# Kernel tuning notes

Hardware: AMD Instinct MI355X
Metric: run time of the kernel (lower is better)

The kernel has to match this reference:

```python
import jax, jax.numpy as jnp
import numpy as np

GROUPS = 8
EPS = 1e-5


def group_norm(x, gamma, beta):
    # x: [B,H,W,C]; normalize per group over (H, W, C/g)
    B, H, W, C = x.shape
    g = GROUPS
    xg = x.reshape(B, H, W, g, C // g)
    mean = jnp.mean(xg, axis=(1, 2, 4), keepdims=True)
    var = jnp.var(xg, axis=(1, 2, 4), keepdims=True)
    xg = (xg - mean) / jnp.sqrt(var + EPS)
    return gamma * xg.reshape(B, H, W, C) + beta


def setup_inputs() -> dict:
    key = jax.random.key(0)
    ks = jax.random.split(key, 6)
    B, H, W, C = 8, 64, 64, 128
    s = 1.0 / np.sqrt(C)
    return {
        "x": jax.random.normal(ks[0], (B, H, W, C), jnp.float32),
        "gamma": jnp.ones((C,), jnp.float32),
        "beta": jnp.zeros((C,), jnp.float32),
        "wq": jax.random.normal(ks[1], (C, C), jnp.float32) * s,
        "bq": jnp.zeros((C,), jnp.float32),
        "wk": jax.random.normal(ks[2], (C, C), jnp.float32) * s,
        "bk": jnp.zeros((C,), jnp.float32),
        "wv": jax.random.normal(ks[3], (C, C), jnp.float32) * s,
        "bv": jnp.zeros((C,), jnp.float32),
        "wp": jax.random.normal(ks[4], (C, C), jnp.float32) * s,
        "bp": jnp.zeros((C,), jnp.float32),
    }


def reference(x, gamma, beta, wq, bq, wk, bk, wv, bv, wp, bp):
    B, H, W, C = x.shape
    scale = jnp.asarray(C, jnp.float32) ** -0.5
    xn = group_norm(x, gamma, beta)  # note: residual uses normalized input (as in source)
    N = H * W
    xf = xn.reshape(B, N, C)
    q = xf @ wq + bq
    k = xf @ wk + bk
    v = xf @ wv + bv
    attn = jnp.einsum('bnc,bmc->bnm', q, k) * scale  # [B, N, N]
    attn = jax.nn.softmax(attn, axis=-1)
    out = jnp.einsum('bnm,bmc->bnc', attn, v)
    out = out @ wp + bp
    return (xf + out).reshape(B, H, W, C)
```

## Files before the change

kernel.cpp:

```cpp
#include <hip/hip_runtime.h>
#include <hip/hip_bf16.h>

#define B_ 8
#define N_ 4096
#define C_ 128
#define EPSV 1e-5f
#define SPLIT 2
#define KVB 64

using bf8   = __attribute__((ext_vector_type(8))) short;
using u16x8 = __attribute__((ext_vector_type(8))) ushort;
using f32x4 = __attribute__((ext_vector_type(4))) float;

__device__ __forceinline__ ushort f2b(float f) {
  __hip_bfloat16 h = __float2bfloat16(f);
  return *reinterpret_cast<ushort*>(&h);
}
__device__ __forceinline__ float b2f(ushort u) {
  union { float f; unsigned x; } t; t.x = ((unsigned)u) << 16; return t.f;
}

__device__ __forceinline__ void gll16(const void* g, void* l) {
  __builtin_amdgcn_global_load_lds((const __attribute__((address_space(1))) void*)g,
                                   (__attribute__((address_space(3))) void*)l,
                                   16, 0, 0);
}

__global__ __launch_bounds__(256) void gnw(const float* __restrict__ x,
                                           const float* __restrict__ wq,
                                           const float* __restrict__ wk,
                                           const float* __restrict__ wv,
                                           const float* __restrict__ wp,
                                           float2* __restrict__ part,
                                           ushort* __restrict__ wt) {
  if (blockIdx.y >= 64) {
    const int widx = blockIdx.y - 64;
    const float* w = (widx == 0) ? wq : (widx == 1) ? wk : (widx == 2) ? wv : wp;
    ushort* o = wt + widx * 16384;
    const int r  = blockIdx.x * 16 + (threadIdx.x >> 4);
    const int c0 = (threadIdx.x & 15) << 3;
    const float4 v0 = *reinterpret_cast<const float4*>(w + (size_t)r * C_ + c0);
    const float4 v1 = *reinterpret_cast<const float4*>(w + (size_t)r * C_ + c0 + 4);
    const float vv[8] = {v0.x, v0.y, v0.z, v0.w, v1.x, v1.y, v1.z, v1.w};
    #pragma unroll
    for (int j = 0; j < 8; ++j) {
      const int n = c0 + j;
      const int el = (r & 7) | ((((r >> 3)) ^ (n & 7)) << 3);
      o[(size_t)n * C_ + el] = f2b(vv[j]);
    }
    return;
  }
  const int bg = blockIdx.y;
  const int b = bg >> 3, g = bg & 7;
  const int chunk = blockIdx.x;
  const float* xp = x + (size_t)b * N_ * C_ + g * 16;
  float s = 0.f, s2 = 0.f;
  const int base4 = chunk * 2048;
  for (int i = threadIdx.x; i < 2048; i += 256) {
    const int idx = base4 + i;
    const int n = idx >> 2, c4 = (idx & 3) << 2;
    const float4 v = *reinterpret_cast<const float4*>(xp + (size_t)n * C_ + c4);
    s  += v.x + v.y + v.z + v.w;
    s2 += v.x*v.x + v.y*v.y + v.z*v.z + v.w*v.w;
  }
  #pragma unroll
  for (int off = 32; off; off >>= 1) { s += __shfl_down(s, off); s2 += __shfl_down(s2, off); }
  __shared__ float red[8];
  const int wid = threadIdx.x >> 6;
  if ((threadIdx.x & 63) == 0) { red[wid] = s; red[4 + wid] = s2; }
  __syncthreads();
  if (threadIdx.x == 0)
    part[bg * 8 + chunk] = make_float2(red[0]+red[1]+red[2]+red[3],
                                       red[4]+red[5]+red[6]+red[7]);
}

__device__ __forceinline__ void block_mrs(const float2* part, int b, int tid,
                                          float2* sp, float* mrs) {
  if (tid < 64) sp[tid] = part[b * 64 + tid];
  __syncthreads();
  if (tid < 8) {
    float s = 0.f, s2 = 0.f;
    #pragma unroll
    for (int c = 0; c < 8; ++c) { s += sp[tid*8+c].x; s2 += sp[tid*8+c].y; }
    const float inv = 1.f / 65536.f;
    const float m = s * inv;
    const float var = s2 * inv - m * m;
    mrs[tid*2]   = m;
    mrs[tid*2+1] = rsqrtf(var + EPSV);
  }
  __syncthreads();
}

__global__ __launch_bounds__(256) void qkv_fused(const float* __restrict__ x,
                                                 const float2* __restrict__ part,
                                                 const float* __restrict__ gamma,
                                                 const float* __restrict__ beta,
                                                 const ushort* __restrict__ wt,
                                                 const float* __restrict__ bq,
                                                 const float* __restrict__ bk,
                                                 const float* __restrict__ bv,
                                                 ushort* __restrict__ qb, ushort* __restrict__ kb,
                                                 ushort* __restrict__ vtb,
                                                 ushort* __restrict__ xnb) {
  __shared__ ushort A[64][128];
  __shared__ ushort Bt[128][128];
  __shared__ float2 sp[64];
  __shared__ float mrs[16];
  const int m0 = blockIdx.x * 64;
  const int tid = threadIdx.x;
  const int wid = tid >> 6, lane = tid & 63;
  block_mrs(part, m0 >> 12, tid, sp, mrs);
  for (int i = tid; i < 1024; i += 256) {
    const int row = i >> 4, c = (i & 15) << 3;
    const int grow = m0 + row;
    const float mm = mrs[(c >> 4) * 2], rr = mrs[(c >> 4) * 2 + 1];
    const float4 v0 = *reinterpret_cast<const float4*>(&x[(size_t)grow * C_ + c]);
    const float4 v1 = *reinterpret_cast<const float4*>(&x[(size_t)grow * C_ + c + 4]);
    const float vv[8] = {v0.x, v0.y, v0.z, v0.w, v1.x, v1.y, v1.z, v1.w};
    u16x8 u;
    #pragma unroll
    for (int j = 0; j < 8; ++j)
      u[j] = f2b((vv[j] - mm) * rr * gamma[c+j] + beta[c+j]);
    *reinterpret_cast<u16x8*>(&xnb[(size_t)grow * C_ + c]) = u;
    const int el = ((c >> 3) ^ (row & 7)) << 3;
    *reinterpret_cast<u16x8*>(&A[row][el]) = u;
  }
  const int wm = wid >> 1, wn = wid & 1;
  const int lr = lane & 15, lk = lane >> 4;
  const float qscale = 0.12751749f;

  #pragma unroll 1
  for (int j = 0; j < 3; ++j) {
    const ushort* wtj = wt + j * 16384;
    const float* bias = (j == 0) ? bq : (j == 1) ? bk : bv;
    __syncthreads();
    {
      ushort* bt0 = &Bt[0][0];
      #pragma unroll
      for (int c8 = 0; c8 < 8; ++c8) {
        const int ch = wid * 8 + c8;
        gll16(wtj + ch * 512 + lane * 8, bt0 + ch * 512);
      }
    }
    __syncthreads();
    f32x4 acc[2][4] = {};
    #pragma unroll
    for (int ks = 0; ks < 4; ++ks) {
      const int g0 = ks * 4 + lk;
      bf8 af[2], bfv[4];
      #pragma unroll
      for (int mi = 0; mi < 2; ++mi) {
        const int row = wm * 32 + mi * 16 + lr;
        af[mi] = *reinterpret_cast<const bf8*>(&A[row][(g0 ^ (row & 7)) << 3]);
      }
      #pragma unroll
      for (int ni = 0; ni < 4; ++ni) {
        const int n = wn * 64 + ni * 16 + lr;
        bfv[ni] = *reinterpret_cast<const bf8*>(&Bt[n][(g0 ^ (n & 7)) << 3]);
      }
      #pragma unroll
      for (int mi = 0; mi < 2; ++mi)
        #pragma unroll
        for (int ni = 0; ni < 4; ++ni)
          acc[mi][ni] = __builtin_amdgcn_mfma_f32_16x16x32_bf16(af[mi], bfv[ni], acc[mi][ni], 0, 0, 0);
    }
    if (j < 2) {
      ushort* out = (j == 0) ? qb : kb;
      const float sc = (j == 0) ? qscale : 1.0f;
      #pragma unroll
      for (int mi = 0; mi < 2; ++mi)
        #pragma unroll
        for (int ni = 0; ni < 4; ++ni)
          #pragma unroll
          for (int r = 0; r < 4; ++r) {
            const int row = m0 + wm * 32 + mi * 16 + lk * 4 + r;
            const int col = wn * 64 + ni * 16 + lr;
            out[(size_t)row * C_ + col] = f2b((acc[mi][ni][r] + bias[col]) * sc);
          }
    } else {
      #pragma unroll
      for (int mi = 0; mi < 2; ++mi)
        #pragma unroll
        for (int ni = 0; ni < 4; ++ni) {
          const int rowb = m0 + wm * 32 + mi * 16 + lk * 4;
          const int col  = wn * 64 + ni * 16 + lr;
          const int bb = rowb >> 12, nn = rowb & 4095;
          const int o  = nn & 63;
          const int op = (o & 0x23) | ((o & 0x0C) << 1) | ((o & 0x10) >> 2);
          const int nnp = (nn & ~63) | op;
          const float bv2 = bias[col];
          ushort4 u;
          u.x = f2b(acc[mi][ni][0] + bv2);
          u.y = f2b(acc[mi][ni][1] + bv2);
          u.z = f2b(acc[mi][ni][2] + bv2);
          u.w = f2b(acc[mi][ni][3] + bv2);
          *reinterpret_cast<ushort4*>(&vtb[((size_t)bb * C_ + col) * N_ + nnp]) = u;
        }
    }
  }
}

__global__ __launch_bounds__(256, 2) void attn_fwd(const ushort* __restrict__ q,
                                                   const ushort* __restrict__ k,
                                                   const ushort* __restrict__ vt,
                                                   ushort* __restrict__ Op,
                                                   float* __restrict__ lsum) {
  extern __shared__ ushort smem[];
  const int bid = blockIdx.x;
  const int b   = bid & 7;
  const int qi  = (bid >> 3) & 31;
  const int z   = bid >> 8;
  const int q0  = qi * 128;
  const int tid = threadIdx.x;
  const int w = tid >> 6, lane = tid & 63;
  const int lr = lane & 15, lk = lane >> 4;
  const ushort* qb = q  + (size_t)b * N_ * C_;
  const ushort* kb = k  + (size_t)b * N_ * C_;
  const ushort* vb = vt + (size_t)b * C_ * N_;

  bf8 qf[2][4];
  #pragma unroll
  for (int h = 0; h < 2; ++h) {
    const int qrow = q0 + w * 32 + h * 16 + lr;
    #pragma unroll
    for (int ks = 0; ks < 4; ++ks)
      qf[h][ks] = *reinterpret_cast<const bf8*>(&qb[(size_t)qrow * C_ + ks * 32 + lk * 8]);
  }

  bf8 onesf;
  #pragma unroll
  for (int j = 0; j < 8; ++j) onesf[j] = (short)0x3F80;

  f32x4 oacc[2][8] = {};
  f32x4 accl[2] = {};

  const int t0 = z * 32;
  const int t1 = t0 + 32;

  const ushort* kg[4];
  const ushort* vg[4];
  #pragma unroll
  for (int j = 0; j < 4; ++j) {
    const int m = w * 4 + j;
    const int krow = m * 4 + (lane >> 4);
    kg[j] = kb + (size_t)(t0 * KVB + krow) * C_ + (((lane & 15) ^ (krow & 7)) << 3);
    const int vrow = m * 8 + (lane >> 3);
    vg[j] = vb + (size_t)vrow * N_ + t0 * KVB + (((lane & 7) ^ (vrow & 7)) << 3);
  }

  auto STAGE = [&](int sel) {
    ushort* Kd = smem + sel * 8192;
    ushort* Vd = smem + 16384 + sel * 8192;
    #pragma unroll
    for (int j = 0; j < 4; ++j) {
      const int m = w * 4 + j;
      gll16(kg[j], Kd + m * 512);
      gll16(vg[j], Vd + m * 512);
    }
    #pragma unroll
    for (int j = 0; j < 4; ++j) { kg[j] += KVB * C_; vg[j] += KVB; }
  };

  STAGE(0);
  __builtin_amdgcn_s_setprio(1);
  #pragma unroll 1
  for (int kt = t0; kt < t1; ++kt) {
    const int cur = (kt - t0) & 1;
    __syncthreads();
    if (kt + 1 < t1) STAGE(cur ^ 1);

    const ushort* Kc = smem + cur * 8192;
    const ushort* Vc = smem + 16384 + cur * 8192;

    f32x4 s[2][4] = {};
    #pragma unroll
    for (int ks = 0; ks < 4; ++ks) {
      const int g0 = ks * 4 + lk;
      bf8 kf[4];
      #pragma unroll
      for (int ni = 0; ni < 4; ++ni) {
        const int n = ni * 16 + lr;
        kf[ni] = *reinterpret_cast<const bf8*>(&Kc[n * 128 + ((g0 ^ (n & 7)) << 3)]);
      }
      #pragma unroll
      for (int h = 0; h < 2; ++h)
        #pragma unroll
        for (int ni = 0; ni < 4; ++ni)
          s[h][ni] = __builtin_amdgcn_mfma_f32_16x16x32_bf16(kf[ni], qf[h][ks], s[h][ni], 0, 0, 0);
    }

    bf8 pa[2][2];
    #pragma unroll
    for (int kss = 0; kss < 2; ++kss)
      #pragma unroll
      for (int h = 0; h < 2; ++h) {
        bf8 t;
        #pragma unroll
        for (int hi = 0; hi < 2; ++hi) {
          const f32x4 sv = s[h][kss * 2 + hi];
          #pragma unroll
          for (int r = 0; r < 4; ++r)
            t[hi * 4 + r] = (short)f2b(__builtin_amdgcn_exp2f(sv[r]));
        }
        pa[kss][h] = t;
      }
    #pragma unroll
    for (int kss = 0; kss < 2; ++kss)
      #pragma unroll
      for (int h = 0; h < 2; ++h)
        accl[h] = __builtin_amdgcn_mfma_f32_16x16x32_bf16(pa[kss][h], onesf, accl[h], 0, 0, 0);

    bf8 vf[8];
    #pragma unroll
    for (int ni = 0; ni < 8; ++ni) {
      const int d = ni * 16 + lr;
      vf[ni] = *reinterpret_cast<const bf8*>(&Vc[d * 64 + ((lk ^ (d & 7)) << 3)]);
    }
    #pragma unroll
    for (int kss = 0; kss < 2; ++kss) {
      #pragma unroll
      for (int h = 0; h < 2; ++h)
        #pragma unroll
        for (int ni = 0; ni < 8; ++ni)
          oacc[h][ni] = __builtin_amdgcn_mfma_f32_16x16x32_bf16(pa[kss][h], vf[ni], oacc[h][ni], 0, 0, 0);
      if (kss == 0) {
        #pragma unroll
        for (int ni = 0; ni < 8; ++ni) {
          const int d = ni * 16 + lr;
          vf[ni] = *reinterpret_cast<const bf8*>(&Vc[d * 64 + (((4 + lk) ^ (d & 7)) << 3)]);
        }
      }
    }
  }
  __builtin_amdgcn_s_setprio(0);

  const size_t zb = (size_t)(z * B_ + b);
  if (lr == 0) {
    #pragma unroll
    for (int h = 0; h < 2; ++h)
      #pragma unroll
      for (int r = 0; r < 4; ++r)
        lsum[zb * N_ + q0 + w * 32 + h * 16 + lk * 4 + r] = accl[h][r];
  }
  ushort* ob = Op + zb * N_ * C_;
  #pragma unroll
  for (int h = 0; h < 2; ++h)
    #pragma unroll
    for (int ni = 0; ni < 8; ++ni)
      #pragma unroll
      for (int r = 0; r < 4; ++r) {
        const int row = q0 + w * 32 + h * 16 + lk * 4 + r;
        ob[(size_t)row * C_ + ni * 16 + lr] = f2b(oacc[h][ni][r]);
      }
}

__global__ __launch_bounds__(256) void proj_res(const ushort* __restrict__ Op,
                                                const float* __restrict__ lsum,
                                                const ushort* __restrict__ wtp,
                                                const float* __restrict__ bias,
                                                const ushort* __restrict__ xnb,
                                                float* __restrict__ outp) {
  __shared__ ushort A[64][128];
  __shared__ ushort Bt[128][128];
  const int m0 = blockIdx.x * 64;
  const int tid = threadIdx.x;
  const int wid = tid >> 6, lane = tid & 63;
  const size_t BN = (size_t)B_ * N_;
  {
    ushort* bt0 = &Bt[0][0];
    #pragma unroll
    for (int c8 = 0; c8 < 8; ++c8) {
      const int ch = wid * 8 + c8;
      gll16(wtp + ch * 512 + lane * 8, bt0 + ch * 512);
    }
  }
  for (int i = tid; i < 1024; i += 256) {
    const int row = i >> 4, c = (i & 15) << 3;
    const size_t grow = m0 + row;
    float l = 0.f;
    #pragma unroll
    for (int zz = 0; zz < SPLIT; ++zz) l += lsum[zz * BN + grow];
    const float inv = 1.f / l;
    float acc8[8] = {};
    #pragma unroll
    for (int zz = 0; zz < SPLIT; ++zz) {
      const u16x8 a = *reinterpret_cast<const u16x8*>(&Op[(zz * BN + grow) * C_ + c]);
      #pragma unroll
      for (int j = 0; j < 8; ++j) acc8[j] += b2f(a[j]);
    }
    u16x8 u;
    #pragma unroll
    for (int j = 0; j < 8; ++j) u[j] = f2b(acc8[j] * inv);
    const int el = ((c >> 3) ^ (row & 7)) << 3;
    *reinterpret_cast<u16x8*>(&A[row][el]) = u;
  }
  __syncthreads();
  const int wm = wid >> 1, wn = wid & 1;
  const int lr = lane & 15, lk = lane >> 4;
  f32x4 acc[2][4] = {};
  #pragma unroll
  for (int ks = 0; ks < 4; ++ks) {
    const int g0 = ks * 4 + lk;
    bf8 af[2], bfv[4];
    #pragma unroll
    for (int mi = 0; mi < 2; ++mi) {
      const int row = wm * 32 + mi * 16 + lr;
      af[mi] = *reinterpret_cast<const bf8*>(&A[row][(g0 ^ (row & 7)) << 3]);
    }
    #pragma unroll
    for (int ni = 0; ni < 4; ++ni) {
      const int n = wn * 64 + ni * 16 + lr;
      bfv[ni] = *reinterpret_cast<const bf8*>(&Bt[n][(g0 ^ (n & 7)) << 3]);
    }
    #pragma unroll
    for (int mi = 0; mi < 2; ++mi)
      #pragma unroll
      for (int ni = 0; ni < 4; ++ni)
        acc[mi][ni] = __builtin_amdgcn_mfma_f32_16x16x32_bf16(af[mi], bfv[ni], acc[mi][ni], 0, 0, 0);
  }
  #pragma unroll
  for (int mi = 0; mi < 2; ++mi)
    #pragma unroll
    for (int ni = 0; ni < 4; ++ni) {
      const int col = wn * 64 + ni * 16 + lr;
      const float bia = bias[col];
      #pragma unroll
      for (int r = 0; r < 4; ++r) {
        const int row = m0 + wm * 32 + mi * 16 + lk * 4 + r;
        const float xn = b2f(xnb[(size_t)row * C_ + col]);
        outp[(size_t)row * C_ + col] = xn + acc[mi][ni][r] + bia;
      }
    }
}

extern "C" void kernel_launch(void* const* d_in, const int* in_sizes, int n_in,
                              void* d_out, int out_size, void* d_ws, size_t ws_size,
                              hipStream_t stream) {
  const float* x     = (const float*)d_in[0];
  const float* gamma = (const float*)d_in[1];
  const float* beta  = (const float*)d_in[2];
  const float* wq    = (const float*)d_in[3];
  const float* bq    = (const float*)d_in[4];
  const float* wk    = (const float*)d_in[5];
  const float* bk    = (const float*)d_in[6];
  const float* wv    = (const float*)d_in[7];
  const float* bv    = (const float*)d_in[8];
  const float* wp    = (const float*)d_in[9];
  const float* bp    = (const float*)d_in[10];
  float* outp = (float*)d_out;

  char* ws = (char*)d_ws;
  const size_t MB8 = (size_t)B_ * N_ * C_ * 2;
  float2* part = (float2*)(ws + 512);
  ushort* qb   = (ushort*)(ws + 8192);
  ushort* kb   = (ushort*)(ws + 8192 + MB8);
  ushort* vtb  = (ushort*)(ws + 8192 + 2*MB8);
  ushort* Op   = (ushort*)(ws + 8192 + 3*MB8);
  float*  lsum = (float*)(ws + 8192 + (3 + SPLIT)*MB8);
  ushort* wt   = (ushort*)(ws + 8192 + (3 + SPLIT)*MB8 + (size_t)SPLIT*B_*N_*4);
  ushort* xnb  = (ushort*)(ws + 8192 + (3 + SPLIT)*MB8 + (size_t)SPLIT*B_*N_*4
                           + 4 * 16384 * sizeof(ushort));

  gnw<<<dim3(8, 68), 256, 0, stream>>>(x, wq, wk, wv, wp, part, wt);
  qkv_fused<<<512, 256, 0, stream>>>(x, part, gamma, beta, wt,
                                     bq, bk, bv, qb, kb, vtb, xnb);
  (void)hipFuncSetAttribute((const void*)attn_fwd,
                            hipFuncAttributeMaxDynamicSharedMemorySize, 65536);
  attn_fwd<<<dim3(32 * B_ * SPLIT), 256, 65536, stream>>>(qb, kb, vtb, Op, lsum);
  proj_res<<<512, 256, 0, stream>>>(Op, lsum, wt + 3 * 16384, bp, xnb, outp);
}
```

Measured before the change: 96.41 us.

## Shrink attention KV tile, split keys three ways, stage output via LDS

The attention kernel now uses 32-key tiles with half the LDS per stage, targets three blocks per CU, and splits the key range into three parts instead of two so more blocks are in flight. The V-transpose permutation in the QKV kernel and the LDS swizzle for V are rewritten to match the 32-wide tiles. Output tiles are written through a swizzled LDS buffer so the global stores are 16-byte and coalesced. The trade-off is more synchronisation per key, more partial results for proj_res to combine, and tighter register limits.

```diff
diff --git a/kernel.cpp b/kernel.cpp
--- a/kernel.cpp
+++ b/kernel.cpp
@@ -5,8 +5,8 @@
 #define N_ 4096
 #define C_ 128
 #define EPSV 1e-5f
-#define SPLIT 2
-#define KVB 64
+#define SPLIT 3
+#define KVB 32
 
 using bf8   = __attribute__((ext_vector_type(8))) short;
 using u16x8 = __attribute__((ext_vector_type(8))) ushort;
@@ -185,9 +185,9 @@
           const int rowb = m0 + wm * 32 + mi * 16 + lk * 4;
           const int col  = wn * 64 + ni * 16 + lr;
           const int bb = rowb >> 12, nn = rowb & 4095;
-          const int o  = nn & 63;
-          const int op = (o & 0x23) | ((o & 0x0C) << 1) | ((o & 0x10) >> 2);
-          const int nnp = (nn & ~63) | op;
+          const int o  = nn & 31;
+          const int op = (o & 3) | ((o & 0x0C) << 1) | ((o & 0x10) >> 2);
+          const int nnp = (nn & ~31) | op;
           const float bv2 = bias[col];
           ushort4 u;
           u.x = f2b(acc[mi][ni][0] + bv2);
@@ -200,7 +200,7 @@
   }
 }
 
-__global__ __launch_bounds__(256, 2) void attn_fwd(const ushort* __restrict__ q,
+__global__ __launch_bounds__(256, 3) void attn_fwd(const ushort* __restrict__ q,
                                                    const ushort* __restrict__ k,
                                                    const ushort* __restrict__ vt,
                                                    ushort* __restrict__ Op,
@@ -234,31 +234,34 @@
   f32x4 oacc[2][8] = {};
   f32x4 accl[2] = {};
 
-  const int t0 = z * 32;
-  const int t1 = t0 + 32;
-
-  const ushort* kg[4];
-  const ushort* vg[4];
-  #pragma unroll
-  for (int j = 0; j < 4; ++j) {
-    const int m = w * 4 + j;
+  const int t0 = (z * 128) / SPLIT;
+  const int t1 = ((z + 1) * 128) / SPLIT;
+
+  const ushort* kg[2];
+  const ushort* vg[2];
+  #pragma unroll
+  for (int j = 0; j < 2; ++j) {
+    const int m = w * 2 + j;
     const int krow = m * 4 + (lane >> 4);
     kg[j] = kb + (size_t)(t0 * KVB + krow) * C_ + (((lane & 15) ^ (krow & 7)) << 3);
-    const int vrow = m * 8 + (lane >> 3);
-    vg[j] = vb + (size_t)vrow * N_ + t0 * KVB + (((lane & 7) ^ (vrow & 7)) << 3);
+    const int dd = m * 8 + (lane >> 3);
+    const int sl = lane & 7;
+    const int d  = dd * 2 + (sl >> 2);
+    const int g  = (sl & 3) ^ (dd & 3);
+    vg[j] = vb + (size_t)d * N_ + t0 * KVB + g * 8;
   }
 
   auto STAGE = [&](int sel) {
-    ushort* Kd = smem + sel * 8192;
-    ushort* Vd = smem + 16384 + sel * 8192;
-    #pragma unroll
-    for (int j = 0; j < 4; ++j) {
-      const int m = w * 4 + j;
+    ushort* Kd = smem + sel * 4096;
+    ushort* Vd = smem + 8192 + sel * 4096;
+    #pragma unroll
+    for (int j = 0; j < 2; ++j) {
+      const int m = w * 2 + j;
       gll16(kg[j], Kd + m * 512);
       gll16(vg[j], Vd + m * 512);
     }
     #pragma unroll
-    for (int j = 0; j < 4; ++j) { kg[j] += KVB * C_; vg[j] += KVB; }
+    for (int j = 0; j < 2; ++j) { kg[j] += KVB * C_; vg[j] += KVB; }
   };
 
   STAGE(0);
@@ -269,67 +272,51 @@
     __syncthreads();
     if (kt + 1 < t1) STAGE(cur ^ 1);
 
-    const ushort* Kc = smem + cur * 8192;
-    const ushort* Vc = smem + 16384 + cur * 8192;
-
-    f32x4 s[2][4] = {};
+    const ushort* Kc = smem + cur * 4096;
+    const ushort* Vc = smem + 8192 + cur * 4096;
+
+    f32x4 s[2][2] = {};
     #pragma unroll
     for (int ks = 0; ks < 4; ++ks) {
       const int g0 = ks * 4 + lk;
-      bf8 kf[4];
-      #pragma unroll
-      for (int ni = 0; ni < 4; ++ni) {
+      bf8 kf[2];
+      #pragma unroll
+      for (int ni = 0; ni < 2; ++ni) {
         const int n = ni * 16 + lr;
         kf[ni] = *reinterpret_cast<const bf8*>(&Kc[n * 128 + ((g0 ^ (n & 7)) << 3)]);
       }
       #pragma unroll
       for (int h = 0; h < 2; ++h)
         #pragma unroll
-        for (int ni = 0; ni < 4; ++ni)
+        for (int ni = 0; ni < 2; ++ni)
           s[h][ni] = __builtin_amdgcn_mfma_f32_16x16x32_bf16(kf[ni], qf[h][ks], s[h][ni], 0, 0, 0);
     }
 
-    bf8 pa[2][2];
-    #pragma unroll
-    for (int kss = 0; kss < 2; ++kss)
-      #pragma unroll
-      for (int h = 0; h < 2; ++h) {
-        bf8 t;
+    bf8 pa[2];
+    #pragma unroll
+    for (int h = 0; h < 2; ++h) {
+      bf8 t;
+      #pragma unroll
+      for (int hi = 0; hi < 2; ++hi) {
+        const f32x4 sv = s[h][hi];
         #pragma unroll
-        for (int hi = 0; hi < 2; ++hi) {
-          const f32x4 sv = s[h][kss * 2 + hi];
-          #pragma unroll
-          for (int r = 0; r < 4; ++r)
-            t[hi * 4 + r] = (short)f2b(__builtin_amdgcn_exp2f(sv[r]));
-        }
-        pa[kss][h] = t;
-      }
-    #pragma unroll
-    for (int kss = 0; kss < 2; ++kss)
-      #pragma unroll
-      for (int h = 0; h < 2; ++h)
-        accl[h] = __builtin_amdgcn_mfma_f32_16x16x32_bf16(pa[kss][h], onesf, accl[h], 0, 0, 0);
-
-    bf8 vf[8];
+        for (int r = 0; r < 4; ++r)
+          t[hi * 4 + r] = (short)f2b(__builtin_amdgcn_exp2f(sv[r]));
+      }
+      pa[h] = t;
+    }
+    #pragma unroll
+    for (int h = 0; h < 2; ++h)
+      accl[h] = __builtin_amdgcn_mfma_f32_16x16x32_bf16(pa[h], onesf, accl[h], 0, 0, 0);
+
     #pragma unroll
     for (int ni = 0; ni < 8; ++ni) {
       const int d = ni * 16 + lr;
-      vf[ni] = *reinterpret_cast<const bf8*>(&Vc[d * 64 + ((lk ^ (d & 7)) << 3)]);
-    }
-    #pragma unroll
-    for (int kss = 0; kss < 2; ++kss) {
+      const int off = (d >> 1) * 64 + ((((d & 1) << 2) | (lk ^ ((d >> 1) & 3))) << 3);
+      const bf8 vf = *reinterpret_cast<const bf8*>(&Vc[off]);
       #pragma unroll
       for (int h = 0; h < 2; ++h)
-        #pragma unroll
-        for (int ni = 0; ni < 8; ++ni)
-          oacc[h][ni] = __builtin_amdgcn_mfma_f32_16x16x32_bf16(pa[kss][h], vf[ni], oacc[h][ni], 0, 0, 0);
-      if (kss == 0) {
-        #pragma unroll
-        for (int ni = 0; ni < 8; ++ni) {
-          const int d = ni * 16 + lr;
-          vf[ni] = *reinterpret_cast<const bf8*>(&Vc[d * 64 + (((4 + lk) ^ (d & 7)) << 3)]);
-        }
-      }
+        oacc[h][ni] = __builtin_amdgcn_mfma_f32_16x16x32_bf16(pa[h], vf, oacc[h][ni], 0, 0, 0);
     }
   }
   __builtin_amdgcn_s_setprio(0);
@@ -342,16 +329,28 @@
       for (int r = 0; r < 4; ++r)
         lsum[zb * N_ + q0 + w * 32 + h * 16 + lk * 4 + r] = accl[h][r];
   }
-  ushort* ob = Op + zb * N_ * C_;
+
+  __syncthreads();
   #pragma unroll
   for (int h = 0; h < 2; ++h)
     #pragma unroll
-    for (int ni = 0; ni < 8; ++ni)
+    for (int ni = 0; ni < 8; ++ni) {
+      const int gc = ni * 2 + (lr >> 3);
       #pragma unroll
       for (int r = 0; r < 4; ++r) {
-        const int row = q0 + w * 32 + h * 16 + lk * 4 + r;
-        ob[(size_t)row * C_ + ni * 16 + lr] = f2b(oacc[h][ni][r]);
-      }
+        const int row = w * 32 + h * 16 + lk * 4 + r;
+        smem[row * 128 + ((gc ^ (row & 7)) << 3) + (lr & 7)] = f2b(oacc[h][ni][r]);
+      }
+    }
+  __syncthreads();
+  ushort* ob = Op + zb * N_ * C_ + (size_t)q0 * C_;
+  #pragma unroll
+  for (int p = 0; p < 8; ++p) {
+    const int i = p * 256 + tid;
+    const int row = i >> 4, g = i & 15;
+    const u16x8 v = *reinterpret_cast<const u16x8*>(&smem[row * 128 + ((g ^ (row & 7)) << 3)]);
+    *reinterpret_cast<u16x8*>(&ob[(size_t)row * C_ + g * 8]) = v;
+  }
 }
 
 __global__ __launch_bounds__(256) void proj_res(const ushort* __restrict__ Op,
@@ -465,7 +464,7 @@
   qkv_fused<<<512, 256, 0, stream>>>(x, part, gamma, beta, wt,
                                      bq, bk, bv, qb, kb, vtb, xnb);
   (void)hipFuncSetAttribute((const void*)attn_fwd,
-                            hipFuncAttributeMaxDynamicSharedMemorySize, 65536);
-  attn_fwd<<<dim3(32 * B_ * SPLIT), 256, 65536, stream>>>(qb, kb, vtb, Op, lsum);
+                            hipFuncAttributeMaxDynamicSharedMemorySize, 32768);
+  attn_fwd<<<dim3(32 * B_ * SPLIT), 256, 32768, stream>>>(qb, kb, vtb, Op, lsum);
   proj_res<<<512, 256, 0, stream>>>(Op, lsum, wt + 3 * 16384, bp, xnb, outp);
 }
```

Result: slower. 99.97 us (+3.7%).
